# Performance work log

Hardware: AMD Instinct MI355X
Metric: run time of the kernel (lower is better)

## Reference

```python
import jax
jax.config.update("jax_enable_x64", True)  # hash primes * indices overflow int32
import jax.numpy as jnp
import numpy as np

HASH_SIZE = 2 ** 19
DIM = 32
CELL_SIZE = 1.0
N = 2_000_000
PRIME_X = 73856093
PRIME_Y = 19349663


def setup_inputs() -> dict:
    key = jax.random.key(0)
    k_pos, k_tab = jax.random.split(key)
    # uniform [0,1) scaled to cover many grid cells (cell_size = 1.0)
    positions = jax.random.uniform(k_pos, (N, 2), dtype=jnp.float32) * 4096.0
    # each slot initialized like torch.randn(dim) * 0.01
    table = jax.random.normal(k_tab, (HASH_SIZE, DIM), dtype=jnp.float32) * 0.01
    return {"positions": positions, "table": table}


def _hash_positions(positions):
    # quantize to integer cell coords, then spatial hash (batch_lookup math)
    ij = jnp.floor(positions / CELL_SIZE).astype(jnp.int64)  # [N,2]
    ix, iy = ij[:, 0], ij[:, 1]
    return jnp.mod(jnp.bitwise_xor(ix * PRIME_X, iy * PRIME_Y), HASH_SIZE)


def reference(positions, table):
    hashed = _hash_positions(positions)          # [N] int64 in [0, HASH_SIZE)
    return jnp.take(table, hashed, axis=0)       # [N, DIM] gather
```

## Files before the change

kernel.cpp:

```cpp
#include <hip/hip_runtime.h>


#define HASH_MASK ((1u << 19) - 1u)
#define SLICE_SHIFT 15
#define NSLICE 16
#define BLOCK 512
#define CHUNK 512

typedef float vfloat2 __attribute__((ext_vector_type(2)));
typedef float vfloat4 __attribute__((ext_vector_type(4)));

__global__ __launch_bounds__(BLOCK) void HashGrid2D_37383395344981_kernel(
    const vfloat2* __restrict__ pos,
    const vfloat4* __restrict__ table,
    vfloat4* __restrict__ out,
    int n)
{
    __shared__ unsigned cnt[NSLICE];
    __shared__ unsigned sbase[NSLICE];
    __shared__ unsigned perm[CHUNK];

    const int tid = threadIdx.x;
    const int r0 = blockIdx.x * CHUNK;
    const int r = r0 + tid;
    const bool valid = (r < n);

    if (tid < NSLICE) cnt[tid] = 0u;
    __syncthreads();

    unsigned h = 0u, rank = 0u;
    if (valid) {
        vfloat2 p = __builtin_nontemporal_load(&pos[r]);
        unsigned ix = (unsigned)(int)floorf(p.x);
        unsigned iy = (unsigned)(int)floorf(p.y);
        h = ((ix * 73856093u) ^ (iy * 19349663u)) & HASH_MASK;
        rank = atomicAdd(&cnt[h >> SLICE_SHIFT], 1u);
    }
    __syncthreads();

    if (tid == 0) {
        unsigned acc = 0u;
#pragma unroll
        for (int s = 0; s < NSLICE; ++s) { sbase[s] = acc; acc += cnt[s]; }
    }
    __syncthreads();

    if (valid) perm[sbase[h >> SLICE_SHIFT] + rank] = (h << 9) | (unsigned)tid;
    __syncthreads();

    const int nrow = (n - r0 < CHUNK) ? (n - r0) : CHUNK;
    const int c = tid & 7;
    const int ri = tid >> 3;
    vfloat4* obase = out + (size_t)r0 * 8;
#pragma unroll 8
    for (int j = 0; j < CHUNK / 64; ++j) {
        int i = ri + 64 * j;
        if (i < nrow) {
            unsigned e = perm[i];
            unsigned hh = e >> 9;
            unsigned lr = e & 511u;
            vfloat4 v = table[(size_t)hh * 8 + c];
            obase[(size_t)lr * 8 + c] = v;
        }
    }
}

extern "C" void kernel_launch(void* const* d_in, const int* in_sizes, int n_in,
                              void* d_out, int out_size, void* d_ws, size_t ws_size,
                              hipStream_t stream) {
    const vfloat2* pos   = (const vfloat2*)d_in[0];
    const vfloat4* table = (const vfloat4*)d_in[1];
    vfloat4* out = (vfloat4*)d_out;

    int n = in_sizes[0] / 2;
    int grid = (n + CHUNK - 1) / CHUNK;

    HashGrid2D_37383395344981_kernel<<<grid, BLOCK, 0, stream>>>(pos, table, out, n);
}
```

Baseline: 333.0 us.

## Persistent blocks sweep table slices in lockstep with cooperative slice prefetch

The kernel becomes persistent: 768 blocks each handle up to six 512-row chunks and process all their rows one 4 MB table slice at a time. While gathering slice s, every block issues global_load_lds prefetches of its assigned share of slice s+1 into a throwaway LDS scratch buffer, so the whole grid warms the cache for the next slice. Output stores become nontemporal. This aims to keep the working set of table rows cache-resident and cut scattered DRAM traffic, at the cost of more LDS use, looser lockstep between blocks, and redundant prefetch loads.

```diff
diff --git a/kernel.cpp b/kernel.cpp
--- a/kernel.cpp
+++ b/kernel.cpp
@@ -6,61 +6,98 @@
 #define NSLICE 16
 #define BLOCK 512
 #define CHUNK 512
+#define GRID 768
+#define KMAX 6
+#define SLICE_BYTES (4u << 20)
+#define SHARE_BYTES 43680u
 
 typedef float vfloat2 __attribute__((ext_vector_type(2)));
 typedef float vfloat4 __attribute__((ext_vector_type(4)));
 
-__global__ __launch_bounds__(BLOCK) void HashGrid2D_37383395344981_kernel(
+__global__ __launch_bounds__(BLOCK, 6) void HashGrid2D_37383395344981_kernel(
     const vfloat2* __restrict__ pos,
     const vfloat4* __restrict__ table,
     vfloat4* __restrict__ out,
-    int n)
+    int n, int nchunks)
 {
-    __shared__ unsigned cnt[NSLICE];
-    __shared__ unsigned sbase[NSLICE];
-    __shared__ unsigned perm[CHUNK];
+    __shared__ unsigned perm[KMAX][CHUNK];
+    __shared__ unsigned cnt[KMAX][NSLICE];
+    __shared__ unsigned sbase[KMAX][NSLICE + 1];
+    __shared__ unsigned scratch[256];
 
     const int tid = threadIdx.x;
-    const int r0 = blockIdx.x * CHUNK;
-    const int r = r0 + tid;
-    const bool valid = (r < n);
+    const int bid = blockIdx.x;
 
-    if (tid < NSLICE) cnt[tid] = 0u;
+    for (int i = tid; i < KMAX * NSLICE; i += BLOCK)
+        ((unsigned*)cnt)[i] = 0u;
     __syncthreads();
 
-    unsigned h = 0u, rank = 0u;
-    if (valid) {
-        vfloat2 p = __builtin_nontemporal_load(&pos[r]);
-        unsigned ix = (unsigned)(int)floorf(p.x);
-        unsigned iy = (unsigned)(int)floorf(p.y);
-        h = ((ix * 73856093u) ^ (iy * 19349663u)) & HASH_MASK;
-        rank = atomicAdd(&cnt[h >> SLICE_SHIFT], 1u);
+    unsigned hv[KMAX], rk[KMAX];
+#pragma unroll
+    for (int k = 0; k < KMAX; ++k) {
+        int c = k * GRID + bid;
+        long long r = (long long)c * CHUNK + tid;
+        hv[k] = 0xFFFFFFFFu;
+        if (c < nchunks && r < n) {
+            vfloat2 p = __builtin_nontemporal_load(&pos[r]);
+            unsigned ix = (unsigned)(int)floorf(p.x);
+            unsigned iy = (unsigned)(int)floorf(p.y);
+            unsigned h = ((ix * 73856093u) ^ (iy * 19349663u)) & HASH_MASK;
+            hv[k] = h;
+            rk[k] = atomicAdd(&cnt[k][h >> SLICE_SHIFT], 1u);
+        }
     }
     __syncthreads();
 
-    if (tid == 0) {
+    if (tid < KMAX) {
         unsigned acc = 0u;
 #pragma unroll
-        for (int s = 0; s < NSLICE; ++s) { sbase[s] = acc; acc += cnt[s]; }
+        for (int s = 0; s < NSLICE; ++s) { sbase[tid][s] = acc; acc += cnt[tid][s]; }
+        sbase[tid][NSLICE] = acc;
     }
     __syncthreads();
 
-    if (valid) perm[sbase[h >> SLICE_SHIFT] + rank] = (h << 9) | (unsigned)tid;
+#pragma unroll
+    for (int k = 0; k < KMAX; ++k)
+        if (hv[k] != 0xFFFFFFFFu)
+            perm[k][sbase[k][hv[k] >> SLICE_SHIFT] + rk[k]] =
+                (hv[k] << 9) | (unsigned)tid;
     __syncthreads();
 
-    const int nrow = (n - r0 < CHUNK) ? (n - r0) : CHUNK;
-    const int c = tid & 7;
+    const int cc = tid & 7;
     const int ri = tid >> 3;
-    vfloat4* obase = out + (size_t)r0 * 8;
-#pragma unroll 8
-    for (int j = 0; j < CHUNK / 64; ++j) {
-        int i = ri + 64 * j;
-        if (i < nrow) {
-            unsigned e = perm[i];
-            unsigned hh = e >> 9;
-            unsigned lr = e & 511u;
-            vfloat4 v = table[(size_t)hh * 8 + c];
-            obase[(size_t)lr * 8 + c] = v;
+    const char* tbytes = (const char*)table;
+
+    for (unsigned s = 0; s < NSLICE; ++s) {
+        if (s + 1 < NSLICE) {
+            unsigned share = ((unsigned)(bid >> 3) + (unsigned)(bid & 7) * 12u) % 96u;
+            size_t sb   = (size_t)(s + 1) * SLICE_BYTES;
+            size_t off  = sb + (size_t)share * SHARE_BYTES;
+            size_t send = sb + SLICE_BYTES;
+            for (int it = 0; it < 6; ++it) {
+                size_t a = off + (size_t)it * (BLOCK * 16) + (size_t)tid * 16;
+                if (a + 16 <= send) {
+                    __builtin_amdgcn_global_load_lds(
+                        (const __attribute__((address_space(1))) unsigned*)(tbytes + a),
+                        (__attribute__((address_space(3))) unsigned*)scratch,
+                        16, 0, 0);
+                }
+            }
+        }
+
+#pragma unroll
+        for (int k = 0; k < KMAX; ++k) {
+            int c = k * GRID + bid;
+            if (c >= nchunks) break;
+            unsigned i1 = sbase[k][s + 1];
+            size_t obase = (size_t)c * CHUNK * 8;
+            for (unsigned i = sbase[k][s] + ri; i < i1; i += 64) {
+                unsigned e = perm[k][i];
+                unsigned hh = e >> 9;
+                unsigned lr = e & 511u;
+                vfloat4 v = table[(size_t)hh * 8 + cc];
+                __builtin_nontemporal_store(v, &out[obase + (size_t)lr * 8 + cc]);
+            }
         }
     }
 }
@@ -73,7 +110,8 @@
     vfloat4* out = (vfloat4*)d_out;
 
     int n = in_sizes[0] / 2;
-    int grid = (n + CHUNK - 1) / CHUNK;
+    int nchunks = (n + CHUNK - 1) / CHUNK;
+    int grid = (nchunks < GRID) ? nchunks : GRID;
 
-    HashGrid2D_37383395344981_kernel<<<grid, BLOCK, 0, stream>>>(pos, table, out, n);
+    HashGrid2D_37383395344981_kernel<<<grid, BLOCK, 0, stream>>>(pos, table, out, n, nchunks);
 }
```

New measurement: 383.4 us. +15.1%, slower.
